# Performance work log

Hardware: AMD Instinct MI355X
Metric: run time of the kernel (lower is better)

Reference implementation:

```python
import jax, jax.numpy as jnp
import numpy as np

B, C, H, W = 32, 3, 128, 128
OH, OW = 32, 32
N = OH * OW


def calc_mask(mu_x, mu_y, sigma_x, sigma_y):
    # Gaussian receptive-field mask, normalized per neuron over (C,H,W) and
    # rescaled by sqrt(C*H*W), as in AdaptiveLocal2DLayer.calc_U (channel_separate=False,
    # normed=True). The mask is identical across channels, so we keep it [H,W,N]
    # and fold the channel count C into the normalization.
    xg = jnp.linspace(0.0, 1.0, W)
    yg = jnp.linspace(0.0, 1.0, H)
    gx = jnp.exp(-0.5 * ((xg[:, None] - mu_x[None, :]) / sigma_x[None, :]) ** 2)  # [W,N]
    gy = jnp.exp(-0.5 * ((yg[:, None] - mu_y[None, :]) / sigma_y[None, :]) ** 2)  # [H,N]
    g = gy[:, None, :] * gx[None, :, :]  # [H,W,N]
    sumsq = C * jnp.sum(g * g, axis=(0, 1), keepdims=True)  # per-neuron sum over C,H,W
    return g / jnp.sqrt(sumsq) * jnp.sqrt(jnp.asarray(C * H * W, dtype=g.dtype))


def setup_inputs() -> dict:
    key = jax.random.key(0)
    kx, kw = jax.random.split(key)
    x = jax.random.normal(kx, (B, C, H, W), dtype=jnp.float32)
    # mu_init='spread': grid of centers with margin 0.2 (np.meshgrid default 'xy')
    margin = 0.2
    grid_y, grid_x = jnp.meshgrid(
        jnp.linspace(margin, 1.0 - margin, OH),
        jnp.linspace(margin, 1.0 - margin, OW),
        indexing='xy')
    mu_x = grid_x.flatten().astype(jnp.float32)
    mu_y = grid_y.flatten().astype(jnp.float32)
    sigma_x = jnp.full((N,), 0.1, dtype=jnp.float32)
    sigma_y = jnp.full((N,), 0.1, dtype=jnp.float32)
    # weight init as in the module: uniform(-bound, bound) with
    # bound = gain*sqrt(6/(eff_fan_in + fan_out)), eff_fan_in = sum(mask^2)
    mask = calc_mask(mu_x, mu_y, sigma_x, sigma_y)
    eff_fan_in = C * jnp.sum(mask ** 2)
    gain = float(np.sqrt(2.0))  # calculate_gain('relu')
    bound = gain * jnp.sqrt(6.0 / (eff_fan_in + N))
    weights = jax.random.uniform(kw, (C, H, W, N), minval=-bound, maxval=bound,
                                 dtype=jnp.float32)
    return {"x": x, "mu_x": mu_x, "mu_y": mu_y,
            "sigma_x": sigma_x, "sigma_y": sigma_y, "weights": weights}


def reference(x, mu_x, mu_y, sigma_x, sigma_y, weights):
    # forward: weighted_mask = mask * weights; tensordot over (C,H,W)
    mask = calc_mask(mu_x, mu_y, sigma_x, sigma_y)  # [H,W,N]
    wm = mask[None, :, :, :] * weights               # [C,H,W,N]
    out = jnp.einsum('bchw,chwn->bn', x, wm)         # [B,N]
    return out.reshape(x.shape[0], 1, OH, OW)
```

## Files before the change

kernel.cpp:

```cpp
#include <hip/hip_runtime.h>
#include <stdint.h>

#define BB 32
#define CC 3
#define HH 128
#define WW 128
#define NN 1024
#define KK (CC*HH*WW)
#define NROWS (CC*HH)
#define KSR NROWS
#define BH 16
#define BSPLIT (BB/BH)
#define NF4 (NN/4)
#define WCH 4
#define NCH (WW/WCH)
#define SG 8
#define STEP (1.0f/127.0f)

__global__ void scale_kernel(const float* __restrict__ mu_x,
                             const float* __restrict__ mu_y,
                             const float* __restrict__ sigma_x,
                             const float* __restrict__ sigma_y,
                             float* __restrict__ scale) {
    int n = blockIdx.x * blockDim.x + threadIdx.x;
    if (n >= NN) return;
    float mux = mu_x[n], muy = mu_y[n];
    float isx = 1.0f / sigma_x[n], isy = 1.0f / sigma_y[n];
    float Sx = 0.f, Sy = 0.f;
    for (int i = 0; i < WW; ++i) {
        float dx = (i * STEP - mux) * isx;
        Sx += __expf(-dx * dx);
        float dy = (i * STEP - muy) * isy;
        Sy += __expf(-dy * dy);
    }
    scale[n] = sqrtf((float)(HH * WW) / (Sx * Sy));
}

__global__ void table_kernel(const float* __restrict__ mu_x,
                             const float* __restrict__ mu_y,
                             const float* __restrict__ sigma_x,
                             const float* __restrict__ sigma_y,
                             const float* __restrict__ scale,
                             float* __restrict__ gxt,
                             float* __restrict__ gyt) {
    int id = blockIdx.x * blockDim.x + threadIdx.x;
    int n = id & (NN - 1);
    int i = id >> 10;
    float sx = sigma_x[n], sy = sigma_y[n];
    float dx = i * STEP - mu_x[n];
    float dy = i * STEP - mu_y[n];
    gxt[id] = __expf(-0.5f * dx * dx / (sx * sx));
    gyt[id] = __expf(-0.5f * dy * dy / (sy * sy)) * scale[n];
}

__global__ __launch_bounds__(256) void main_pipe(
    const float* __restrict__ weights,
    const float* __restrict__ x,
    const float* __restrict__ gyt,
    const float* __restrict__ mu_x,
    const float* __restrict__ sigma_x,
    float* __restrict__ part)
{
    __shared__ float wbuf[4][2][WCH][256];
    __shared__ float xtile[WW][BH];
    const int tid  = threadIdx.x;
    const int wv   = tid >> 6;
    const int lane = tid & 63;

    const int d    = blockIdx.x;
    const int xcd  = d & 7;
    const int slot = d >> 3;
    const int g    = xcd * (KSR / 8) + (slot >> 1);
    const int b0   = (slot & 1) * BH;
    const int r    = g;
    const int h    = r & (HH - 1);

    {
        const int b = tid & (BH - 1);
        const int c = tid >> 4;
        const float* xp = x + (size_t)(b0 + b) * KK + (size_t)r * WW + c * 8;
        const float4 v0 = ((const float4*)xp)[0];
        const float4 v1 = ((const float4*)xp)[1];
        const int w = c * 8;
        xtile[w+0][b] = v0.x; xtile[w+1][b] = v0.y;
        xtile[w+2][b] = v0.z; xtile[w+3][b] = v0.w;
        xtile[w+4][b] = v1.x; xtile[w+5][b] = v1.y;
        xtile[w+6][b] = v1.z; xtile[w+7][b] = v1.w;
    }

    const float4 mux = ((const float4*)mu_x)[tid];
    const float4 sx  = ((const float4*)sigma_x)[tid];
    float4 ax, axs, Bf;
    ax.x = -0.5f/(sx.x*sx.x); ax.y = -0.5f/(sx.y*sx.y);
    ax.z = -0.5f/(sx.z*sx.z); ax.w = -0.5f/(sx.w*sx.w);
    axs.x = ax.x*STEP; axs.y = ax.y*STEP; axs.z = ax.z*STEP; axs.w = ax.w*STEP;
    Bf.x = __expf(2.f*axs.x*STEP); Bf.y = __expf(2.f*axs.y*STEP);
    Bf.z = __expf(2.f*axs.z*STEP); Bf.w = __expf(2.f*axs.w*STEP);

    const float4 gyrow = ((const float4*)(gyt + (size_t)h * NN))[tid];

    const float* wrow = weights + (size_t)r * WW * NN + wv * 256 + lane * 4;
    auto stage = [&](int c) {
        const float* gsrc = wrow + (size_t)(c * WCH) * NN;
        float* lb = &wbuf[wv][c & 1][0][0];
#pragma unroll
        for (int i = 0; i < WCH; ++i) {
            __builtin_amdgcn_global_load_lds(
                (const __attribute__((address_space(1))) unsigned int*)(gsrc + (size_t)i * NN),
                (__attribute__((address_space(3))) unsigned int*)(lb + i * 256),
                16, 0, 0);
        }
    };

    __syncthreads();
    stage(0);

    float4 acc[BH];
#pragma unroll
    for (int b = 0; b < BH; ++b) acc[b] = make_float4(0.f, 0.f, 0.f, 0.f);

    float4 g4, r4;
    for (int c = 0; c < NCH; ++c) {
        if (c + 1 < NCH) stage(c + 1);

        if ((c & 3) == 0) {
            const float w0s = (float)(c * WCH) * STEP;
            float dd;
            dd = w0s - mux.x; g4.x = __expf(ax.x*dd*dd)*gyrow.x; r4.x = __expf(axs.x*(2.f*dd+STEP));
            dd = w0s - mux.y; g4.y = __expf(ax.y*dd*dd)*gyrow.y; r4.y = __expf(axs.y*(2.f*dd+STEP));
            dd = w0s - mux.z; g4.z = __expf(ax.z*dd*dd)*gyrow.z; r4.z = __expf(axs.z*(2.f*dd+STEP));
            dd = w0s - mux.w; g4.w = __expf(ax.w*dd*dd)*gyrow.w; r4.w = __expf(axs.w*(2.f*dd+STEP));
        }

        if (c + 1 < NCH) {
            asm volatile("s_waitcnt vmcnt(4)" ::: "memory");
        } else {
            asm volatile("s_waitcnt vmcnt(0)" ::: "memory");
        }
        __builtin_amdgcn_sched_barrier(0);

        const float* wb = &wbuf[wv][c & 1][0][0];
        const int w0 = c * WCH;
#pragma unroll
        for (int i = 0; i < WCH; ++i) {
            const float4 wt = *(const float4*)(wb + i * 256 + (lane << 2));
            const float4* tr = (const float4*)&xtile[w0 + i][0];
            float4 t;
            t.x = g4.x * wt.x; t.y = g4.y * wt.y;
            t.z = g4.z * wt.z; t.w = g4.w * wt.w;
#pragma unroll
            for (int q = 0; q < 4; ++q) {
                const float4 xv = tr[q];
                acc[4*q+0].x = fmaf(xv.x, t.x, acc[4*q+0].x);
                acc[4*q+0].y = fmaf(xv.x, t.y, acc[4*q+0].y);
                acc[4*q+0].z = fmaf(xv.x, t.z, acc[4*q+0].z);
                acc[4*q+0].w = fmaf(xv.x, t.w, acc[4*q+0].w);
                acc[4*q+1].x = fmaf(xv.y, t.x, acc[4*q+1].x);
                acc[4*q+1].y = fmaf(xv.y, t.y, acc[4*q+1].y);
                acc[4*q+1].z = fmaf(xv.y, t.z, acc[4*q+1].z);
                acc[4*q+1].w = fmaf(xv.y, t.w, acc[4*q+1].w);
                acc[4*q+2].x = fmaf(xv.z, t.x, acc[4*q+2].x);
                acc[4*q+2].y = fmaf(xv.z, t.y, acc[4*q+2].y);
                acc[4*q+2].z = fmaf(xv.z, t.z, acc[4*q+2].z);
                acc[4*q+2].w = fmaf(xv.z, t.w, acc[4*q+2].w);
                acc[4*q+3].x = fmaf(xv.w, t.x, acc[4*q+3].x);
                acc[4*q+3].y = fmaf(xv.w, t.y, acc[4*q+3].y);
                acc[4*q+3].z = fmaf(xv.w, t.z, acc[4*q+3].z);
                acc[4*q+3].w = fmaf(xv.w, t.w, acc[4*q+3].w);
            }
            g4.x *= r4.x; g4.y *= r4.y; g4.z *= r4.z; g4.w *= r4.w;
            r4.x *= Bf.x; r4.y *= Bf.y; r4.z *= Bf.z; r4.w *= Bf.w;
        }
    }

    float* pp = part + ((size_t)g * BB + b0) * NN + (tid << 2);
#pragma unroll
    for (int b = 0; b < BH; ++b)
        *(float4*)(pp + (size_t)b * NN) = acc[b];
}

__global__ __launch_bounds__(256) void reduce1_kernel(const float* __restrict__ part,
                                                      float* __restrict__ part2) {
    const int sg = blockIdx.x >> 5;
    const int cq = (blockIdx.x & 31) * 256 + threadIdx.x;
    const int s0 = sg * (KSR / SG);
    float4 a = make_float4(0.f, 0.f, 0.f, 0.f);
#pragma unroll 4
    for (int s = 0; s < KSR / SG; ++s) {
        const float4 v = *(const float4*)(part + (size_t)(s0 + s) * (BB * NN) + cq * 4);
        a.x += v.x; a.y += v.y; a.z += v.z; a.w += v.w;
    }
    *(float4*)(part2 + ((size_t)sg * (BB * NN) + cq * 4)) = a;
}

__global__ __launch_bounds__(256) void reduce2_kernel(const float* __restrict__ part2,
                                                      float* __restrict__ out) {
    const int cq = blockIdx.x * 256 + threadIdx.x;
    float4 a = make_float4(0.f, 0.f, 0.f, 0.f);
#pragma unroll
    for (int sgi = 0; sgi < SG; ++sgi) {
        const float4 v = *(const float4*)(part2 + (size_t)sgi * (BB * NN) + cq * 4);
        a.x += v.x; a.y += v.y; a.z += v.z; a.w += v.w;
    }
    *(float4*)(out + cq * 4) = a;
}

template <int MODE>
__global__ __launch_bounds__(256) void main_fallback(
    const float* __restrict__ weights,
    const float* __restrict__ x,
    const float* __restrict__ gxt,
    const float* __restrict__ gyt,
    const float* __restrict__ mu_x, const float* __restrict__ mu_y,
    const float* __restrict__ sigma_x, const float* __restrict__ sigma_y,
    float* __restrict__ dst)
{
    __shared__ float tile[2][WW][8];
    const int tid = threadIdx.x;
    const int g   = blockIdx.x;
    const int b0  = blockIdx.y * 8;
    const int r0  = g * 2;

    {
        const int b = tid & 7;
        const int c = tid >> 3;
        const float* xp = x + (size_t)(b0 + b) * KK + (size_t)r0 * WW + c * 8;
        const float4 v0 = ((const float4*)xp)[0];
        const float4 v1 = ((const float4*)xp)[1];
        const int row = (c * 8) >> 7;
        const int w   = (c * 8) & (WW - 1);
        tile[row][w+0][b] = v0.x; tile[row][w+1][b] = v0.y;
        tile[row][w+2][b] = v0.z; tile[row][w+3][b] = v0.w;
        tile[row][w+4][b] = v1.x; tile[row][w+5][b] = v1.y;
        tile[row][w+6][b] = v1.z; tile[row][w+7][b] = v1.w;
    }

    float4 mux4, ax4, ay4, muy4, sc4;
    if constexpr (MODE == 2) {
        mux4 = ((const float4*)mu_x)[tid];
        muy4 = ((const float4*)mu_y)[tid];
        float4 sx4 = ((const float4*)sigma_x)[tid];
        float4 sy4 = ((const float4*)sigma_y)[tid];
        ax4.x=-0.5f/(sx4.x*sx4.x); ax4.y=-0.5f/(sx4.y*sx4.y);
        ax4.z=-0.5f/(sx4.z*sx4.z); ax4.w=-0.5f/(sx4.w*sx4.w);
        ay4.x=-0.5f/(sy4.x*sy4.x); ay4.y=-0.5f/(sy4.y*sy4.y);
        ay4.z=-0.5f/(sy4.z*sy4.z); ay4.w=-0.5f/(sy4.w*sy4.w);
        float Sx[4]={0,0,0,0}, Sy[4]={0,0,0,0};
        for (int i = 0; i < WW; ++i) {
            float pp = i * STEP, dd;
            dd=pp-mux4.x; Sx[0]+=__expf(2.f*ax4.x*dd*dd);
            dd=pp-mux4.y; Sx[1]+=__expf(2.f*ax4.y*dd*dd);
            dd=pp-mux4.z; Sx[2]+=__expf(2.f*ax4.z*dd*dd);
            dd=pp-mux4.w; Sx[3]+=__expf(2.f*ax4.w*dd*dd);
            dd=pp-muy4.x; Sy[0]+=__expf(2.f*ay4.x*dd*dd);
            dd=pp-muy4.y; Sy[1]+=__expf(2.f*ay4.y*dd*dd);
            dd=pp-muy4.z; Sy[2]+=__expf(2.f*ay4.z*dd*dd);
            dd=pp-muy4.w; Sy[3]+=__expf(2.f*ay4.w*dd*dd);
        }
        sc4.x = sqrtf((float)(HH*WW)/(Sx[0]*Sy[0]));
        sc4.y = sqrtf((float)(HH*WW)/(Sx[1]*Sy[1]));
        sc4.z = sqrtf((float)(HH*WW)/(Sx[2]*Sy[2]));
        sc4.w = sqrtf((float)(HH*WW)/(Sx[3]*Sy[3]));
    }
    __syncthreads();

    float acc[8][4];
#pragma unroll
    for (int b = 0; b < 8; ++b)
        acc[b][0] = acc[b][1] = acc[b][2] = acc[b][3] = 0.f;

#pragma unroll
    for (int rr = 0; rr < 2; ++rr) {
        const int rrow = r0 + rr;
        const int hh = rrow & (HH - 1);
        float4 gys;
        if constexpr (MODE == 2) {
            float hp = hh * STEP, dd;
            dd=hp-muy4.x; gys.x = __expf(ay4.x*dd*dd) * sc4.x;
            dd=hp-muy4.y; gys.y = __expf(ay4.y*dd*dd) * sc4.y;
            dd=hp-muy4.z; gys.z = __expf(ay4.z*dd*dd) * sc4.z;
            dd=hp-muy4.w; gys.w = __expf(ay4.w*dd*dd) * sc4.w;
        } else {
            gys = ((const float4*)(gyt + (size_t)hh * NN))[tid];
        }
        const float4* wp  = (const float4*)(weights + (size_t)rrow * WW * NN) + tid;
        const float4* gxp = (const float4*)gxt + tid;
        float racc[8][4];
#pragma unroll
        for (int b = 0; b < 8; ++b)
            racc[b][0] = racc[b][1] = racc[b][2] = racc[b][3] = 0.f;
        auto GX = [&](int w) -> float4 {
            if constexpr (MODE == 2) {
                float pp = w * STEP, dd;
                float4 gg;
                dd=pp-mux4.x; gg.x = __expf(ax4.x*dd*dd);
                dd=pp-mux4.y; gg.y = __expf(ax4.y*dd*dd);
                dd=pp-mux4.z; gg.z = __expf(ax4.z*dd*dd);
                dd=pp-mux4.w; gg.w = __expf(ax4.w*dd*dd);
                return gg;
            } else {
                return gxp[(size_t)w * NF4];
            }
        };
#define COMPUTE(WIDX, WT, GXV)                                          \
        {                                                               \
            float4 t;                                                   \
            t.x = GXV.x * WT.x; t.y = GXV.y * WT.y;                     \
            t.z = GXV.z * WT.z; t.w = GXV.w * WT.w;                     \
            const float4* trp = (const float4*)&tile[rr][WIDX][0];      \
            float xs[8];                                                \
            ((float4*)xs)[0] = trp[0]; ((float4*)xs)[1] = trp[1];       \
            _Pragma("unroll")                                           \
            for (int b = 0; b < 8; ++b) {                               \
                racc[b][0] = fmaf(xs[b], t.x, racc[b][0]);              \
                racc[b][1] = fmaf(xs[b], t.y, racc[b][1]);              \
                racc[b][2] = fmaf(xs[b], t.z, racc[b][2]);              \
                racc[b][3] = fmaf(xs[b], t.w, racc[b][3]);              \
            }                                                           \
        }
        float4 wtA = wp[0];
        float4 gxA = GX(0);
        float4 wtB = wp[NF4];
        float4 gxB = GX(1);
        for (int w = 0; w < WW; w += 2) {
            const int wn = (w + 2 < WW) ? (w + 2) : (WW - 2);
            float4 wtA2 = wp[(size_t)wn * NF4];
            float4 gxA2 = GX(wn);
            float4 wtB2 = wp[(size_t)(wn + 1) * NF4];
            float4 gxB2 = GX(wn + 1);
            COMPUTE(w,     wtA, gxA);
            COMPUTE(w + 1, wtB, gxB);
            wtA = wtA2; gxA = gxA2; wtB = wtB2; gxB = gxB2;
        }
#undef COMPUTE
#pragma unroll
        for (int b = 0; b < 8; ++b) {
            acc[b][0] = fmaf(gys.x, racc[b][0], acc[b][0]);
            acc[b][1] = fmaf(gys.y, racc[b][1], acc[b][1]);
            acc[b][2] = fmaf(gys.z, racc[b][2], acc[b][2]);
            acc[b][3] = fmaf(gys.w, racc[b][3], acc[b][3]);
        }
    }

    float* op = dst + (size_t)b0 * NN + tid * 4;
#pragma unroll
    for (int b = 0; b < 8; ++b) {
        atomicAdd(op + (size_t)b * NN + 0, acc[b][0]);
        atomicAdd(op + (size_t)b * NN + 1, acc[b][1]);
        atomicAdd(op + (size_t)b * NN + 2, acc[b][2]);
        atomicAdd(op + (size_t)b * NN + 3, acc[b][3]);
    }
}

extern "C" void kernel_launch(void* const* d_in, const int* in_sizes, int n_in,
                              void* d_out, int out_size, void* d_ws, size_t ws_size,
                              hipStream_t stream) {
    const float* x       = (const float*)d_in[0];
    const float* mu_x    = (const float*)d_in[1];
    const float* mu_y    = (const float*)d_in[2];
    const float* sigma_x = (const float*)d_in[3];
    const float* sigma_y = (const float*)d_in[4];
    const float* weights = (const float*)d_in[5];
    float* out = (float*)d_out;

    float* scale = (float*)d_ws;
    float* gxt   = (float*)((char*)d_ws + 4096);
    float* gyt   = gxt + (size_t)HH * NN;
    float* part  = gyt + (size_t)HH * NN;
    float* part2 = part + (size_t)KSR * BB * NN;
    const size_t need_tbl  = 4096 + 2 * sizeof(float) * (size_t)HH * NN;
    const size_t need_part = need_tbl +
        sizeof(float) * ((size_t)KSR * BB * NN + (size_t)SG * BB * NN);

    if (ws_size >= need_part) {
        scale_kernel<<<(NN + 255) / 256, 256, 0, stream>>>(mu_x, mu_y, sigma_x, sigma_y, scale);
        table_kernel<<<(HH * NN) / 256, 256, 0, stream>>>(mu_x, mu_y, sigma_x, sigma_y,
                                                          scale, gxt, gyt);
        main_pipe<<<KSR * BSPLIT, 256, 0, stream>>>(weights, x, gyt, mu_x, sigma_x, part);
        reduce1_kernel<<<32 * SG, 256, 0, stream>>>(part, part2);
        reduce2_kernel<<<BB * NN / 4 / 256, 256, 0, stream>>>(part2, out);
    } else if (ws_size >= need_tbl) {
        hipMemsetAsync(d_out, 0, (size_t)out_size * sizeof(float), stream);
        scale_kernel<<<(NN + 255) / 256, 256, 0, stream>>>(mu_x, mu_y, sigma_x, sigma_y, scale);
        table_kernel<<<(HH * NN) / 256, 256, 0, stream>>>(mu_x, mu_y, sigma_x, sigma_y,
                                                          scale, gxt, gyt);
        dim3 grid(NROWS / 2, 4);
        main_fallback<1><<<grid, 256, 0, stream>>>(weights, x, gxt, gyt,
                                                   mu_x, mu_y, sigma_x, sigma_y, out);
    } else {
        hipMemsetAsync(d_out, 0, (size_t)out_size * sizeof(float), stream);
        dim3 grid(NROWS / 2, 4);
        main_fallback<2><<<grid, 256, 0, stream>>>(weights, x, nullptr, nullptr,
                                                   mu_x, mu_y, sigma_x, sigma_y, out);
    }
}
```

Before: 78.91 us.

## Stream weights through registers, pre-transpose x, compute gy inline

```diff
diff --git a/kernel.cpp b/kernel.cpp
--- a/kernel.cpp
+++ b/kernel.cpp
@@ -1,5 +1,4 @@
 #include <hip/hip_runtime.h>
-#include <stdint.h>
 
 #define BB 32
 #define CC 3
@@ -11,7 +10,6 @@
 #define KSR NROWS
 #define BH 16
 #define BSPLIT (BB/BH)
-#define NF4 (NN/4)
 #define WCH 4
 #define NCH (WW/WCH)
 #define SG 8
@@ -36,33 +34,34 @@
     scale[n] = sqrtf((float)(HH * WW) / (Sx * Sy));
 }
 
-__global__ void table_kernel(const float* __restrict__ mu_x,
-                             const float* __restrict__ mu_y,
-                             const float* __restrict__ sigma_x,
-                             const float* __restrict__ sigma_y,
-                             const float* __restrict__ scale,
-                             float* __restrict__ gxt,
-                             float* __restrict__ gyt) {
-    int id = blockIdx.x * blockDim.x + threadIdx.x;
-    int n = id & (NN - 1);
-    int i = id >> 10;
-    float sx = sigma_x[n], sy = sigma_y[n];
-    float dx = i * STEP - mu_x[n];
-    float dy = i * STEP - mu_y[n];
-    gxt[id] = __expf(-0.5f * dx * dx / (sx * sx));
-    gyt[id] = __expf(-0.5f * dy * dy / (sy * sy)) * scale[n];
+__global__ void xpose_kernel(const float* __restrict__ x, float* __restrict__ xT) {
+    __shared__ float tile[64][BB + 1];
+    int k0 = blockIdx.x * 64;
+    int lane = threadIdx.x & 63;
+    int bgrp = threadIdx.x >> 6;
+#pragma unroll
+    for (int i = 0; i < 8; ++i) {
+        int b = bgrp * 8 + i;
+        tile[lane][b] = x[(size_t)b * KK + k0 + lane];
+    }
+    __syncthreads();
+    int b = threadIdx.x & 31;
+    int kk0 = threadIdx.x >> 5;
+#pragma unroll
+    for (int i = 0; i < 8; ++i) {
+        int kk = i * 8 + kk0;
+        xT[(size_t)(k0 + kk) * BB + b] = tile[kk][b];
+    }
 }
 
 __global__ __launch_bounds__(256) void main_pipe(
     const float* __restrict__ weights,
-    const float* __restrict__ x,
-    const float* __restrict__ gyt,
-    const float* __restrict__ mu_x,
-    const float* __restrict__ sigma_x,
+    const float* __restrict__ xT,
+    const float* __restrict__ scale,
+    const float* __restrict__ mu_x, const float* __restrict__ mu_y,
+    const float* __restrict__ sigma_x, const float* __restrict__ sigma_y,
     float* __restrict__ part)
 {
-    __shared__ float wbuf[4][2][WCH][256];
-    __shared__ float xtile[WW][BH];
     const int tid  = threadIdx.x;
     const int wv   = tid >> 6;
     const int lane = tid & 63;
@@ -74,104 +73,107 @@
     const int b0   = (slot & 1) * BH;
     const int r    = g;
     const int h    = r & (HH - 1);
-
-    {
-        const int b = tid & (BH - 1);
-        const int c = tid >> 4;
-        const float* xp = x + (size_t)(b0 + b) * KK + (size_t)r * WW + c * 8;
-        const float4 v0 = ((const float4*)xp)[0];
-        const float4 v1 = ((const float4*)xp)[1];
-        const int w = c * 8;
-        xtile[w+0][b] = v0.x; xtile[w+1][b] = v0.y;
-        xtile[w+2][b] = v0.z; xtile[w+3][b] = v0.w;
-        xtile[w+4][b] = v1.x; xtile[w+5][b] = v1.y;
-        xtile[w+6][b] = v1.z; xtile[w+7][b] = v1.w;
-    }
-
-    const float4 mux = ((const float4*)mu_x)[tid];
-    const float4 sx  = ((const float4*)sigma_x)[tid];
-    float4 ax, axs, Bf;
-    ax.x = -0.5f/(sx.x*sx.x); ax.y = -0.5f/(sx.y*sx.y);
-    ax.z = -0.5f/(sx.z*sx.z); ax.w = -0.5f/(sx.w*sx.w);
+    const int nq   = wv * 64 + lane;
+
+    const float4 mux = ((const float4*)mu_x)[nq];
+    const float4 sx4 = ((const float4*)sigma_x)[nq];
+    const float4 muy = ((const float4*)mu_y)[nq];
+    const float4 sy4 = ((const float4*)sigma_y)[nq];
+    const float4 sc4 = ((const float4*)scale)[nq];
+
+    float4 ax, axs, Bf, gyrow;
+    ax.x = -0.5f/(sx4.x*sx4.x); ax.y = -0.5f/(sx4.y*sx4.y);
+    ax.z = -0.5f/(sx4.z*sx4.z); ax.w = -0.5f/(sx4.w*sx4.w);
     axs.x = ax.x*STEP; axs.y = ax.y*STEP; axs.z = ax.z*STEP; axs.w = ax.w*STEP;
     Bf.x = __expf(2.f*axs.x*STEP); Bf.y = __expf(2.f*axs.y*STEP);
     Bf.z = __expf(2.f*axs.z*STEP); Bf.w = __expf(2.f*axs.w*STEP);
-
-    const float4 gyrow = ((const float4*)(gyt + (size_t)h * NN))[tid];
-
-    const float* wrow = weights + (size_t)r * WW * NN + wv * 256 + lane * 4;
-    auto stage = [&](int c) {
-        const float* gsrc = wrow + (size_t)(c * WCH) * NN;
-        float* lb = &wbuf[wv][c & 1][0][0];
-#pragma unroll
-        for (int i = 0; i < WCH; ++i) {
-            __builtin_amdgcn_global_load_lds(
-                (const __attribute__((address_space(1))) unsigned int*)(gsrc + (size_t)i * NN),
-                (__attribute__((address_space(3))) unsigned int*)(lb + i * 256),
-                16, 0, 0);
-        }
+    {
+        const float hp = h * STEP;
+        float ayc, dd;
+        ayc = -0.5f/(sy4.x*sy4.x); dd = hp-muy.x; gyrow.x = __expf(ayc*dd*dd)*sc4.x;
+        ayc = -0.5f/(sy4.y*sy4.y); dd = hp-muy.y; gyrow.y = __expf(ayc*dd*dd)*sc4.y;
+        ayc = -0.5f/(sy4.z*sy4.z); dd = hp-muy.z; gyrow.z = __expf(ayc*dd*dd)*sc4.z;
+        ayc = -0.5f/(sy4.w*sy4.w); dd = hp-muy.w; gyrow.w = __expf(ayc*dd*dd)*sc4.w;
+    }
+
+    const float* wbase = weights + (size_t)r * WW * NN + nq * 4;
+    const float4* xr4  = (const float4*)xT + (size_t)r * (WW * BB / 4) + (b0 >> 2);
+
+    float4 wR[2][4];
+#define WLOAD(BUF, C)                                                   \
+    {                                                                   \
+        _Pragma("unroll")                                               \
+        for (int i = 0; i < 4; ++i)                                     \
+            wR[BUF][i] = *(const float4*)(wbase + (size_t)((C)*WCH + i) * NN); \
+    }
+
+    float4 acc[BH];
+#pragma unroll
+    for (int b = 0; b < BH; ++b) acc[b] = make_float4(0.f, 0.f, 0.f, 0.f);
+
+    float4 g4, r4;
+    auto resync = [&](int w0) {
+        const float w0s = (float)w0 * STEP;
+        float dd;
+        dd = w0s - mux.x; g4.x = __expf(ax.x*dd*dd)*gyrow.x; r4.x = __expf(axs.x*(2.f*dd+STEP));
+        dd = w0s - mux.y; g4.y = __expf(ax.y*dd*dd)*gyrow.y; r4.y = __expf(axs.y*(2.f*dd+STEP));
+        dd = w0s - mux.z; g4.z = __expf(ax.z*dd*dd)*gyrow.z; r4.z = __expf(axs.z*(2.f*dd+STEP));
+        dd = w0s - mux.w; g4.w = __expf(ax.w*dd*dd)*gyrow.w; r4.w = __expf(axs.w*(2.f*dd+STEP));
     };
 
-    __syncthreads();
-    stage(0);
-
-    float4 acc[BH];
-#pragma unroll
-    for (int b = 0; b < BH; ++b) acc[b] = make_float4(0.f, 0.f, 0.f, 0.f);
-
-    float4 g4, r4;
-    for (int c = 0; c < NCH; ++c) {
-        if (c + 1 < NCH) stage(c + 1);
-
-        if ((c & 3) == 0) {
-            const float w0s = (float)(c * WCH) * STEP;
-            float dd;
-            dd = w0s - mux.x; g4.x = __expf(ax.x*dd*dd)*gyrow.x; r4.x = __expf(axs.x*(2.f*dd+STEP));
-            dd = w0s - mux.y; g4.y = __expf(ax.y*dd*dd)*gyrow.y; r4.y = __expf(axs.y*(2.f*dd+STEP));
-            dd = w0s - mux.z; g4.z = __expf(ax.z*dd*dd)*gyrow.z; r4.z = __expf(axs.z*(2.f*dd+STEP));
-            dd = w0s - mux.w; g4.w = __expf(ax.w*dd*dd)*gyrow.w; r4.w = __expf(axs.w*(2.f*dd+STEP));
-        }
-
-        if (c + 1 < NCH) {
-            asm volatile("s_waitcnt vmcnt(4)" ::: "memory");
-        } else {
-            asm volatile("s_waitcnt vmcnt(0)" ::: "memory");
-        }
-        __builtin_amdgcn_sched_barrier(0);
-
-        const float* wb = &wbuf[wv][c & 1][0][0];
-        const int w0 = c * WCH;
-#pragma unroll
-        for (int i = 0; i < WCH; ++i) {
-            const float4 wt = *(const float4*)(wb + i * 256 + (lane << 2));
-            const float4* tr = (const float4*)&xtile[w0 + i][0];
-            float4 t;
-            t.x = g4.x * wt.x; t.y = g4.y * wt.y;
-            t.z = g4.z * wt.z; t.w = g4.w * wt.w;
-#pragma unroll
-            for (int q = 0; q < 4; ++q) {
-                const float4 xv = tr[q];
-                acc[4*q+0].x = fmaf(xv.x, t.x, acc[4*q+0].x);
-                acc[4*q+0].y = fmaf(xv.x, t.y, acc[4*q+0].y);
-                acc[4*q+0].z = fmaf(xv.x, t.z, acc[4*q+0].z);
-                acc[4*q+0].w = fmaf(xv.x, t.w, acc[4*q+0].w);
-                acc[4*q+1].x = fmaf(xv.y, t.x, acc[4*q+1].x);
-                acc[4*q+1].y = fmaf(xv.y, t.y, acc[4*q+1].y);
-                acc[4*q+1].z = fmaf(xv.y, t.z, acc[4*q+1].z);
-                acc[4*q+1].w = fmaf(xv.y, t.w, acc[4*q+1].w);
-                acc[4*q+2].x = fmaf(xv.z, t.x, acc[4*q+2].x);
-                acc[4*q+2].y = fmaf(xv.z, t.y, acc[4*q+2].y);
-                acc[4*q+2].z = fmaf(xv.z, t.z, acc[4*q+2].z);
-                acc[4*q+2].w = fmaf(xv.z, t.w, acc[4*q+2].w);
-                acc[4*q+3].x = fmaf(xv.w, t.x, acc[4*q+3].x);
-                acc[4*q+3].y = fmaf(xv.w, t.y, acc[4*q+3].y);
-                acc[4*q+3].z = fmaf(xv.w, t.z, acc[4*q+3].z);
-                acc[4*q+3].w = fmaf(xv.w, t.w, acc[4*q+3].w);
-            }
-            g4.x *= r4.x; g4.y *= r4.y; g4.z *= r4.z; g4.w *= r4.w;
-            r4.x *= Bf.x; r4.y *= Bf.y; r4.z *= Bf.z; r4.w *= Bf.w;
-        }
-    }
+#define FMAQ(XQ, A0)                                                    \
+    {                                                                   \
+        acc[A0+0].x = fmaf(XQ.x, t.x, acc[A0+0].x);                     \
+        acc[A0+0].y = fmaf(XQ.x, t.y, acc[A0+0].y);                     \
+        acc[A0+0].z = fmaf(XQ.x, t.z, acc[A0+0].z);                     \
+        acc[A0+0].w = fmaf(XQ.x, t.w, acc[A0+0].w);                     \
+        acc[A0+1].x = fmaf(XQ.y, t.x, acc[A0+1].x);                     \
+        acc[A0+1].y = fmaf(XQ.y, t.y, acc[A0+1].y);                     \
+        acc[A0+1].z = fmaf(XQ.y, t.z, acc[A0+1].z);                     \
+        acc[A0+1].w = fmaf(XQ.y, t.w, acc[A0+1].w);                     \
+        acc[A0+2].x = fmaf(XQ.z, t.x, acc[A0+2].x);                     \
+        acc[A0+2].y = fmaf(XQ.z, t.y, acc[A0+2].y);                     \
+        acc[A0+2].z = fmaf(XQ.z, t.z, acc[A0+2].z);                     \
+        acc[A0+2].w = fmaf(XQ.z, t.w, acc[A0+2].w);                     \
+        acc[A0+3].x = fmaf(XQ.w, t.x, acc[A0+3].x);                     \
+        acc[A0+3].y = fmaf(XQ.w, t.y, acc[A0+3].y);                     \
+        acc[A0+3].z = fmaf(XQ.w, t.z, acc[A0+3].z);                     \
+        acc[A0+3].w = fmaf(XQ.w, t.w, acc[A0+3].w);                     \
+    }
+
+#define CHUNK(BUF, C)                                                   \
+    {                                                                   \
+        if (((C) & 3) == 0) resync((C) * WCH);                          \
+        _Pragma("unroll")                                               \
+        for (int i = 0; i < 4; ++i) {                                   \
+            const int w = (C) * WCH + i;                                \
+            const float4 xq0 = xr4[w*8 + 0];                            \
+            const float4 xq1 = xr4[w*8 + 1];                            \
+            const float4 xq2 = xr4[w*8 + 2];                            \
+            const float4 xq3 = xr4[w*8 + 3];                            \
+            const float4 wt  = wR[BUF][i];                              \
+            float4 t;                                                   \
+            t.x = g4.x * wt.x; t.y = g4.y * wt.y;                       \
+            t.z = g4.z * wt.z; t.w = g4.w * wt.w;                       \
+            FMAQ(xq0, 0)                                                \
+            FMAQ(xq1, 4)                                                \
+            FMAQ(xq2, 8)                                                \
+            FMAQ(xq3, 12)                                               \
+            g4.x *= r4.x; g4.y *= r4.y; g4.z *= r4.z; g4.w *= r4.w;     \
+            r4.x *= Bf.x; r4.y *= Bf.y; r4.z *= Bf.z; r4.w *= Bf.w;     \
+        }                                                               \
+    }
+
+    WLOAD(0, 0);
+    for (int c = 0; c < NCH; c += 2) {
+        WLOAD(1, c + 1);
+        CHUNK(0, c);
+        if (c + 2 < NCH) WLOAD(0, c + 2);
+        CHUNK(1, c + 1);
+    }
+#undef CHUNK
+#undef FMAQ
+#undef WLOAD
 
     float* pp = part + ((size_t)g * BB + b0) * NN + (tid << 2);
 #pragma unroll
@@ -205,12 +207,9 @@
     *(float4*)(out + cq * 4) = a;
 }
 
-template <int MODE>
 __global__ __launch_bounds__(256) void main_fallback(
     const float* __restrict__ weights,
     const float* __restrict__ x,
-    const float* __restrict__ gxt,
-    const float* __restrict__ gyt,
     const float* __restrict__ mu_x, const float* __restrict__ mu_y,
     const float* __restrict__ sigma_x, const float* __restrict__ sigma_y,
     float* __restrict__ dst)
@@ -235,16 +234,16 @@
         tile[row][w+6][b] = v1.z; tile[row][w+7][b] = v1.w;
     }
 
-    float4 mux4, ax4, ay4, muy4, sc4;
-    if constexpr (MODE == 2) {
-        mux4 = ((const float4*)mu_x)[tid];
-        muy4 = ((const float4*)mu_y)[tid];
-        float4 sx4 = ((const float4*)sigma_x)[tid];
-        float4 sy4 = ((const float4*)sigma_y)[tid];
-        ax4.x=-0.5f/(sx4.x*sx4.x); ax4.y=-0.5f/(sx4.y*sx4.y);
-        ax4.z=-0.5f/(sx4.z*sx4.z); ax4.w=-0.5f/(sx4.w*sx4.w);
-        ay4.x=-0.5f/(sy4.x*sy4.x); ay4.y=-0.5f/(sy4.y*sy4.y);
-        ay4.z=-0.5f/(sy4.z*sy4.z); ay4.w=-0.5f/(sy4.w*sy4.w);
+    float4 mux4 = ((const float4*)mu_x)[tid];
+    float4 muy4 = ((const float4*)mu_y)[tid];
+    float4 sx4  = ((const float4*)sigma_x)[tid];
+    float4 sy4  = ((const float4*)sigma_y)[tid];
+    float4 ax4, ay4, sc4;
+    ax4.x=-0.5f/(sx4.x*sx4.x); ax4.y=-0.5f/(sx4.y*sx4.y);
+    ax4.z=-0.5f/(sx4.z*sx4.z); ax4.w=-0.5f/(sx4.w*sx4.w);
+    ay4.x=-0.5f/(sy4.x*sy4.x); ay4.y=-0.5f/(sy4.y*sy4.y);
+    ay4.z=-0.5f/(sy4.z*sy4.z); ay4.w=-0.5f/(sy4.w*sy4.w);
+    {
         float Sx[4]={0,0,0,0}, Sy[4]={0,0,0,0};
         for (int i = 0; i < WW; ++i) {
             float pp = i * STEP, dd;
@@ -274,65 +273,37 @@
         const int rrow = r0 + rr;
         const int hh = rrow & (HH - 1);
         float4 gys;
-        if constexpr (MODE == 2) {
+        {
             float hp = hh * STEP, dd;
             dd=hp-muy4.x; gys.x = __expf(ay4.x*dd*dd) * sc4.x;
             dd=hp-muy4.y; gys.y = __expf(ay4.y*dd*dd) * sc4.y;
             dd=hp-muy4.z; gys.z = __expf(ay4.z*dd*dd) * sc4.z;
             dd=hp-muy4.w; gys.w = __expf(ay4.w*dd*dd) * sc4.w;
-        } else {
-            gys = ((const float4*)(gyt + (size_t)hh * NN))[tid];
         }
-        const float4* wp  = (const float4*)(weights + (size_t)rrow * WW * NN) + tid;
-        const float4* gxp = (const float4*)gxt + tid;
+        const float4* wp = (const float4*)(weights + (size_t)rrow * WW * NN) + tid;
         float racc[8][4];
 #pragma unroll
         for (int b = 0; b < 8; ++b)
             racc[b][0] = racc[b][1] = racc[b][2] = racc[b][3] = 0.f;
-        auto GX = [&](int w) -> float4 {
-            if constexpr (MODE == 2) {
-                float pp = w * STEP, dd;
-                float4 gg;
-                dd=pp-mux4.x; gg.x = __expf(ax4.x*dd*dd);
-                dd=pp-mux4.y; gg.y = __expf(ax4.y*dd*dd);
-                dd=pp-mux4.z; gg.z = __expf(ax4.z*dd*dd);
-                dd=pp-mux4.w; gg.w = __expf(ax4.w*dd*dd);
-                return gg;
-            } else {
-                return gxp[(size_t)w * NF4];
+        for (int w = 0; w < WW; ++w) {
+            const float4 wt = wp[(size_t)w * (NN/4)];
+            float pp = w * STEP, dd;
+            float4 t;
+            dd=pp-mux4.x; t.x = __expf(ax4.x*dd*dd) * wt.x;
+            dd=pp-mux4.y; t.y = __expf(ax4.y*dd*dd) * wt.y;
+            dd=pp-mux4.z; t.z = __expf(ax4.z*dd*dd) * wt.z;
+            dd=pp-mux4.w; t.w = __expf(ax4.w*dd*dd) * wt.w;
+            const float4* trp = (const float4*)&tile[rr][w][0];
+            float xs[8];
+            ((float4*)xs)[0] = trp[0]; ((float4*)xs)[1] = trp[1];
+#pragma unroll
+            for (int b = 0; b < 8; ++b) {
+                racc[b][0] = fmaf(xs[b], t.x, racc[b][0]);
+                racc[b][1] = fmaf(xs[b], t.y, racc[b][1]);
+                racc[b][2] = fmaf(xs[b], t.z, racc[b][2]);
+                racc[b][3] = fmaf(xs[b], t.w, racc[b][3]);
             }
-        };
-#define COMPUTE(WIDX, WT, GXV)                                          \
-        {                                                               \
-            float4 t;                                                   \
-            t.x = GXV.x * WT.x; t.y = GXV.y * WT.y;                     \
-            t.z = GXV.z * WT.z; t.w = GXV.w * WT.w;                     \
-            const float4* trp = (const float4*)&tile[rr][WIDX][0];      \
-            float xs[8];                                                \
-            ((float4*)xs)[0] = trp[0]; ((float4*)xs)[1] = trp[1];       \
-            _Pragma("unroll")                                           \
-            for (int b = 0; b < 8; ++b) {                               \
-                racc[b][0] = fmaf(xs[b], t.x, racc[b][0]);              \
-                racc[b][1] = fmaf(xs[b], t.y, racc[b][1]);              \
-                racc[b][2] = fmaf(xs[b], t.z, racc[b][2]);              \
-                racc[b][3] = fmaf(xs[b], t.w, racc[b][3]);              \
-            }                                                           \
         }
-        float4 wtA = wp[0];
-        float4 gxA = GX(0);
-        float4 wtB = wp[NF4];
-        float4 gxB = GX(1);
-        for (int w = 0; w < WW; w += 2) {
-            const int wn = (w + 2 < WW) ? (w + 2) : (WW - 2);
-            float4 wtA2 = wp[(size_t)wn * NF4];
-            float4 gxA2 = GX(wn);
-            float4 wtB2 = wp[(size_t)(wn + 1) * NF4];
-            float4 gxB2 = GX(wn + 1);
-            COMPUTE(w,     wtA, gxA);
-            COMPUTE(w + 1, wtB, gxB);
-            wtA = wtA2; gxA = gxA2; wtB = wtB2; gxB = gxB2;
-        }
-#undef COMPUTE
 #pragma unroll
         for (int b = 0; b < 8; ++b) {
             acc[b][0] = fmaf(gys.x, racc[b][0], acc[b][0]);
@@ -364,33 +335,23 @@
     float* out = (float*)d_out;
 
     float* scale = (float*)d_ws;
-    float* gxt   = (float*)((char*)d_ws + 4096);
-    float* gyt   = gxt + (size_t)HH * NN;
-    float* part  = gyt + (size_t)HH * NN;
+    float* xT    = (float*)((char*)d_ws + 4096);
+    float* part  = xT + (size_t)KK * BB;
     float* part2 = part + (size_t)KSR * BB * NN;
-    const size_t need_tbl  = 4096 + 2 * sizeof(float) * (size_t)HH * NN;
-    const size_t need_part = need_tbl +
-        sizeof(float) * ((size_t)KSR * BB * NN + (size_t)SG * BB * NN);
-
-    if (ws_size >= need_part) {
+    const size_t need = 4096 +
+        sizeof(float) * ((size_t)KK * BB + (size_t)KSR * BB * NN + (size_t)SG * BB * NN);
+
+    if (ws_size >= need) {
         scale_kernel<<<(NN + 255) / 256, 256, 0, stream>>>(mu_x, mu_y, sigma_x, sigma_y, scale);
-        table_kernel<<<(HH * NN) / 256, 256, 0, stream>>>(mu_x, mu_y, sigma_x, sigma_y,
-                                                          scale, gxt, gyt);
-        main_pipe<<<KSR * BSPLIT, 256, 0, stream>>>(weights, x, gyt, mu_x, sigma_x, part);
+        xpose_kernel<<<KK / 64, 256, 0, stream>>>(x, xT);
+        main_pipe<<<KSR * BSPLIT, 256, 0, stream>>>(weights, xT, scale,
+                                                    mu_x, mu_y, sigma_x, sigma_y, part);
         reduce1_kernel<<<32 * SG, 256, 0, stream>>>(part, part2);
         reduce2_kernel<<<BB * NN / 4 / 256, 256, 0, stream>>>(part2, out);
-    } else if (ws_size >= need_tbl) {
-        hipMemsetAsync(d_out, 0, (size_t)out_size * sizeof(float), stream);
-        scale_kernel<<<(NN + 255) / 256, 256, 0, stream>>>(mu_x, mu_y, sigma_x, sigma_y, scale);
-        table_kernel<<<(HH * NN) / 256, 256, 0, stream>>>(mu_x, mu_y, sigma_x, sigma_y,
-                                                          scale, gxt, gyt);
-        dim3 grid(NROWS / 2, 4);
-        main_fallback<1><<<grid, 256, 0, stream>>>(weights, x, gxt, gyt,
-                                                   mu_x, mu_y, sigma_x, sigma_y, out);
     } else {
         hipMemsetAsync(d_out, 0, (size_t)out_size * sizeof(float), stream);
         dim3 grid(NROWS / 2, 4);
-        main_fallback<2><<<grid, 256, 0, stream>>>(weights, x, nullptr, nullptr,
-                                                   mu_x, mu_y, sigma_x, sigma_y, out);
-    }
-}
+        main_fallback<<<grid, 256, 0, stream>>>(weights, x,
+                                                mu_x, mu_y, sigma_x, sigma_y, out);
+    }
+}
```

New measurement: 74.23 us. -5.9%, faster.
